# Optimization experiments

Hardware: AMD Instinct MI355X
Metric: run time of the kernel (lower is better)

Reference implementation:

```python
import jax, jax.numpy as jnp
import numpy as np

N = 100000   # nodes
E = 1600000  # directed edges
F_IN, F_HID, F_OUT = 10, 64, 4


def setup_inputs() -> dict:
    key = jax.random.key(0)
    ks = jax.random.split(key, 8)
    x = jax.random.normal(ks[0], (N, F_IN), dtype=jnp.float32)
    edge_index = jax.random.randint(ks[1], (2, E), 0, N, dtype=jnp.int64)
    W1 = jax.random.normal(ks[2], (F_IN, F_HID), dtype=jnp.float32) * (1.0 / np.sqrt(F_IN))
    b1 = jnp.zeros((F_HID,), dtype=jnp.float32)
    W2 = jax.random.normal(ks[3], (F_HID, F_HID), dtype=jnp.float32) * (1.0 / np.sqrt(F_HID))
    b2 = jnp.zeros((F_HID,), dtype=jnp.float32)
    W3 = jax.random.normal(ks[4], (F_HID, F_OUT), dtype=jnp.float32) * (1.0 / np.sqrt(F_HID))
    b3 = jnp.zeros((F_OUT,), dtype=jnp.float32)
    return {"x": x, "edge_index": edge_index, "W1": W1, "b1": b1,
            "W2": W2, "b2": b2, "W3": W3, "b3": b3}


def _gcn_layer(h_in, W, b, src, dst, dinv_sqrt):
    # GCNConv: D^{-1/2} (A + I) D^{-1/2} (h_in W) + b, with deg counted incl. self-loops
    h = h_in @ W                                   # [N, F_out]
    norm = dinv_sqrt[src] * dinv_sqrt[dst]         # [E]
    msg = h[src] * norm[:, None]                   # [E, F_out]  (dominant traffic)
    agg = jax.ops.segment_sum(msg, dst, num_segments=N)
    agg = agg + h * (dinv_sqrt * dinv_sqrt)[:, None]  # self-loop contribution
    return agg + b


def reference(x, edge_index, W1, b1, W2, b2, W3, b3):
    src, dst = edge_index[0], edge_index[1]
    # degree of target nodes including self-loop
    deg = jax.ops.segment_sum(jnp.ones((E,), x.dtype), dst, num_segments=N) + 1.0
    dinv_sqrt = jax.lax.rsqrt(deg)
    h = jax.nn.relu(_gcn_layer(x, W1, b1, src, dst, dinv_sqrt))
    # dropout is identity in eval mode (training=False)
    h = jax.nn.relu(_gcn_layer(h, W2, b2, src, dst, dinv_sqrt))
    h = _gcn_layer(h, W3, b3, src, dst, dinv_sqrt)
    return jax.nn.log_softmax(h, axis=1)
```

## Files before the change

### kernel.cpp

```cpp
#include <hip/hip_runtime.h>
#include <hip/hip_bf16.h>
#include <math.h>


#define D_MAX 48
#define BUCK_SH 7
#define NPB 128
#define NBK 782
#define P1_BLOCKS 256
#define P1_THREADS 512
#define SEG_CAP 36

typedef __hip_bfloat16 bf16;

__global__ void k_bin(const int* __restrict__ src, const int* __restrict__ dst,
                      int* __restrict__ arena, int* __restrict__ cnt2, int E) {
    __shared__ int lcnt[NBK];
    int t = threadIdx.x, blk = blockIdx.x;
    for (int i = t; i < NBK; i += P1_THREADS) lcnt[i] = 0;
    __syncthreads();
    int chunk = (E + P1_BLOCKS - 1) / P1_BLOCKS;
    int e0 = blk * chunk;
    int e1 = min(e0 + chunk, E);
    for (int e = e0 + t; e < e1; e += P1_THREADS) {
        int d = __builtin_nontemporal_load(dst + e);
        int s = __builtin_nontemporal_load(src + e);
        int b = d >> BUCK_SH;
        int rec = (d & (NPB - 1)) | (s << BUCK_SH);
        int slot = atomicAdd(&lcnt[b], 1);
        if (slot < SEG_CAP)
            arena[((size_t)b * P1_BLOCKS + blk) * SEG_CAP + slot] = rec;
    }
    __syncthreads();
    for (int b = t; b < NBK; b += P1_THREADS)
        cnt2[b * P1_BLOCKS + blk] = lcnt[b];
}

__global__ void k_ellbuild(const int* __restrict__ arena, const int* __restrict__ cnt2,
                           const float* __restrict__ x,
                           int* __restrict__ ell, int* __restrict__ cnt,
                           float* __restrict__ dinv, bf16* __restrict__ xp, int N) {
    __shared__ int cnt128[NPB];
    __shared__ int ellb[NPB * D_MAX];
    __shared__ float dloc[NPB];
    int t = threadIdx.x, b = blockIdx.x;
    if (t < NPB) cnt128[t] = 0;
    __syncthreads();
    int c = cnt2[b * P1_BLOCKS + t];
    int cc = min(c, SEG_CAP);
    const int* seg = arena + ((size_t)b * P1_BLOCKS + t) * SEG_CAP;
    for (int i = 0; i < cc; ++i) {
        int rec = seg[i];
        int r = rec & (NPB - 1);
        int s = rec >> BUCK_SH;
        int slot = atomicAdd(&cnt128[r], 1);
        if (slot < D_MAX) ellb[r * D_MAX + slot] = s;
    }
    __syncthreads();
    int nb = b << BUCK_SH;
    if (t < NPB) {
        int n = nb + t;
        if (n < N) {
            int dg = cnt128[t];
            cnt[n] = dg;
            float dv = rsqrtf((float)dg + 1.0f);
            dinv[n] = dv;
            dloc[t] = dv;
        }
    }
    __syncthreads();
    for (int i = t; i < NPB * D_MAX; i += 256) {
        int n = nb + i / D_MAX;
        if (n < N) ell[(size_t)nb * D_MAX + i] = ellb[i];
    }
    for (int i = t; i < NPB * 10; i += 256) {
        int n = nb + i / 10;
        if (n < N) xp[(size_t)nb * 10 + i] = __float2bfloat16(x[(size_t)nb * 10 + i] * dloc[i / 10]);
    }
}

__global__ void k_gather10(const int* __restrict__ ell, const int* __restrict__ cnt,
                           const bf16* __restrict__ xp, const float* __restrict__ dinv,
                           float* __restrict__ aggx, int N) {
    int tid = threadIdx.x;
    int g = tid & 15;
    int node = blockIdx.x * 16 + (tid >> 4);
    if (node >= N) return;
    int deg = cnt[node]; if (deg > D_MAX) deg = D_MAX;
    float acc = 0.0f;
    for (int c0 = 0; c0 < deg; c0 += 16) {
        int m = deg - c0; if (m > 16) m = 16;
        int sid = 0;
        if (g < m) sid = ell[(size_t)node * D_MAX + c0 + g];
        for (int i = 0; i < m; ++i) {
            int s = __shfl(sid, i, 16);
            if (g < 10) acc += __bfloat162float(xp[(size_t)s * 10 + g]);
        }
    }
    if (g < 10) {
        acc += __bfloat162float(xp[(size_t)node * 10 + g]);
        aggx[(size_t)node * 10 + g] = dinv[node] * acc;
    }
}

__global__ void k_fused1(const float* __restrict__ aggx, const float* __restrict__ W1,
                         const float* __restrict__ b1, const float* __restrict__ W2,
                         const float* __restrict__ dinv, bf16* __restrict__ t, int N) {
    __shared__ float W1s[10 * 64];
    __shared__ float h1s[64][64];
    int tid = threadIdx.x;
    int f = tid & 63, w = tid >> 6;
    float w2c[64];
#pragma unroll
    for (int k = 0; k < 64; ++k) w2c[k] = W2[k * 64 + f];
    for (int i = tid; i < 640; i += 256) W1s[i] = W1[i];
    __syncthreads();
    int nb = blockIdx.x * 64;
    float bf = b1[f];
    for (int j = 0; j < 16; ++j) {
        int ln = w * 16 + j;
        int n = nb + ln;
        float acc = bf;
        if (n < N) {
#pragma unroll
            for (int k = 0; k < 10; ++k)
                acc = fmaf(aggx[(size_t)n * 10 + k], W1s[k * 64 + f], acc);
        }
        h1s[ln][f] = fmaxf(acc, 0.0f);
    }
    __syncthreads();
    for (int j = 0; j < 16; ++j) {
        int ln = w * 16 + j;
        int n = nb + ln;
        if (n >= N) continue;
        float acc = 0.0f;
        const float4* hr = (const float4*)h1s[ln];
#pragma unroll
        for (int k4 = 0; k4 < 16; ++k4) {
            float4 h = hr[k4];
            acc = fmaf(h.x, w2c[k4 * 4 + 0], acc);
            acc = fmaf(h.y, w2c[k4 * 4 + 1], acc);
            acc = fmaf(h.z, w2c[k4 * 4 + 2], acc);
            acc = fmaf(h.w, w2c[k4 * 4 + 3], acc);
        }
        t[(size_t)n * 64 + f] = __float2bfloat16(acc * dinv[n]);
    }
}

__global__ void k_fused2(const int* __restrict__ ell, const int* __restrict__ cnt,
                         const bf16* __restrict__ t, const float* __restrict__ dinv,
                         const float* __restrict__ b2, const float* __restrict__ W3,
                         float* __restrict__ t3, int N) {
    __shared__ float W3s[256];
    int tid = threadIdx.x;
    W3s[tid] = W3[tid];
    __syncthreads();
    int f = tid & 63;
    int node = blockIdx.x * 4 + (tid >> 6);
    if (node >= N) return;
    int deg = cnt[node]; if (deg > D_MAX) deg = D_MAX;
    int sid = 0;
    if (f < deg) sid = ell[(size_t)node * D_MAX + f];
    float acc = 0.0f;
    int i = 0;
    for (; i + 4 <= deg; i += 4) {
        int s0 = __shfl(sid, i),     s1 = __shfl(sid, i + 1);
        int s2 = __shfl(sid, i + 2), s3 = __shfl(sid, i + 3);
        float v0 = __bfloat162float(t[(size_t)s0 * 64 + f]);
        float v1 = __bfloat162float(t[(size_t)s1 * 64 + f]);
        float v2 = __bfloat162float(t[(size_t)s2 * 64 + f]);
        float v3 = __bfloat162float(t[(size_t)s3 * 64 + f]);
        acc += v0 + v1;
        acc += v2 + v3;
    }
    for (; i < deg; ++i) {
        int s = __shfl(sid, i);
        acc += __bfloat162float(t[(size_t)s * 64 + f]);
    }
    float di = dinv[node];
    acc += __bfloat162float(t[(size_t)node * 64 + f]);
    float h2 = fmaxf(di * acc + b2[f], 0.0f);
    float p0 = h2 * W3s[f * 4 + 0];
    float p1 = h2 * W3s[f * 4 + 1];
    float p2 = h2 * W3s[f * 4 + 2];
    float p3 = h2 * W3s[f * 4 + 3];
#pragma unroll
    for (int off = 32; off > 0; off >>= 1) {
        p0 += __shfl_down(p0, off);
        p1 += __shfl_down(p1, off);
        p2 += __shfl_down(p2, off);
        p3 += __shfl_down(p3, off);
    }
    if (f == 0) {
        float4 r = {p0 * di, p1 * di, p2 * di, p3 * di};
        *(float4*)(t3 + (size_t)node * 4) = r;
    }
}

__global__ void k_out(const int* __restrict__ ell, const int* __restrict__ cnt,
                      const float* __restrict__ t3, const float* __restrict__ dinv,
                      const float* __restrict__ b3, float* __restrict__ out, int N) {
    int n = blockIdx.x * blockDim.x + threadIdx.x;
    if (n >= N) return;
    int deg = cnt[n]; if (deg > D_MAX) deg = D_MAX;
    float a0 = 0.f, a1 = 0.f, a2 = 0.f, a3 = 0.f;
    const int* row = ell + (size_t)n * D_MAX;
    for (int c = 0; c < deg; c += 4) {
        int4 q = *(const int4*)(row + c);
        {
            float4 v = *(const float4*)(t3 + (size_t)q.x * 4);
            a0 += v.x; a1 += v.y; a2 += v.z; a3 += v.w;
        }
        if (c + 1 < deg) {
            float4 v = *(const float4*)(t3 + (size_t)q.y * 4);
            a0 += v.x; a1 += v.y; a2 += v.z; a3 += v.w;
        }
        if (c + 2 < deg) {
            float4 v = *(const float4*)(t3 + (size_t)q.z * 4);
            a0 += v.x; a1 += v.y; a2 += v.z; a3 += v.w;
        }
        if (c + 3 < deg) {
            float4 v = *(const float4*)(t3 + (size_t)q.w * 4);
            a0 += v.x; a1 += v.y; a2 += v.z; a3 += v.w;
        }
    }
    float4 sv = *(const float4*)(t3 + (size_t)n * 4);
    a0 += sv.x; a1 += sv.y; a2 += sv.z; a3 += sv.w;
    float di = dinv[n];
    float v0 = di * a0 + b3[0];
    float v1 = di * a1 + b3[1];
    float v2 = di * a2 + b3[2];
    float v3 = di * a3 + b3[3];
    float m = fmaxf(fmaxf(v0, v1), fmaxf(v2, v3));
    float s = expf(v0 - m) + expf(v1 - m) + expf(v2 - m) + expf(v3 - m);
    float ls = m + logf(s);
    float4 r = {v0 - ls, v1 - ls, v2 - ls, v3 - ls};
    *(float4*)(out + (size_t)n * 4) = r;
}

extern "C" void kernel_launch(void* const* d_in, const int* in_sizes, int n_in,
                              void* d_out, int out_size, void* d_ws, size_t ws_size,
                              hipStream_t stream) {
    const float* x  = (const float*)d_in[0];
    const int*   ei = (const int*)d_in[1];
    const float* W1 = (const float*)d_in[2];
    const float* b1 = (const float*)d_in[3];
    const float* W2 = (const float*)d_in[4];
    const float* b2 = (const float*)d_in[5];
    const float* W3 = (const float*)d_in[6];
    const float* b3 = (const float*)d_in[7];
    float* out = (float*)d_out;

    const int E = in_sizes[1] / 2;
    const int N = in_sizes[0] / 10;
    const int* src = ei;
    const int* dst = ei + E;

    float* dinv  = (float*)d_ws;
    int*   cnt   = (int*)(dinv + N);
    int*   ell   = cnt + N;
    bf16*  xp    = (bf16*)(ell + (size_t)N * D_MAX);
    float* t3    = (float*)(xp + (size_t)N * 10 + 4);
    int*   arena = (int*)(t3 + (size_t)N * 4);
    int*   cnt2  = arena + (size_t)NBK * P1_BLOCKS * SEG_CAP;
    float* aggx  = (float*)arena;
    bf16*  tbuf  = (bf16*)(aggx + (size_t)N * 10);

    k_bin<<<P1_BLOCKS, P1_THREADS, 0, stream>>>(src, dst, arena, cnt2, E);
    k_ellbuild<<<NBK, 256, 0, stream>>>(arena, cnt2, x, ell, cnt, dinv, xp, N);

    k_gather10<<<(N + 15) / 16, 256, 0, stream>>>(ell, cnt, xp, dinv, aggx, N);
    k_fused1<<<(N + 63) / 64, 256, 0, stream>>>(aggx, W1, b1, W2, dinv, tbuf, N);
    k_fused2<<<(N + 3) / 4, 256, 0, stream>>>(ell, cnt, tbuf, dinv, b2, W3, t3, N);
    k_out<<<(N + 255) / 256, 256, 0, stream>>>(ell, cnt, t3, dinv, b3, out, N);
}
```

Before: 199.6 us.

## Fuse layer-1 gather into dense kernel, vectorize binning loads, deepen gather unroll

Merges the 10-feature neighbor gather into the layer-1/layer-2 transform kernel, so the aggregated features stay in shared memory and one launch plus the aggx round trip through global memory go away. The binning pass now reads src/dst as 4-wide vectors, and the ELL build reads segment records as int4. The layer-2 gather loop is unrolled from 4 to 8 neighbors for more memory-level parallelism. The t3 alignment padding changes, and the fused kernel may lose occupancy because the gather now runs inside a register-heavy kernel.

New measurement: 200.5 us. Within noise of the previous version (+0.4%).

```diff
diff --git a/kernel.cpp b/kernel.cpp
--- a/kernel.cpp
+++ b/kernel.cpp
@@ -12,6 +12,7 @@
 #define SEG_CAP 36
 
 typedef __hip_bfloat16 bf16;
+typedef int int4v __attribute__((ext_vector_type(4)));
 
 __global__ void k_bin(const int* __restrict__ src, const int* __restrict__ dst,
                       int* __restrict__ arena, int* __restrict__ cnt2, int E) {
@@ -19,18 +20,30 @@
     int t = threadIdx.x, blk = blockIdx.x;
     for (int i = t; i < NBK; i += P1_THREADS) lcnt[i] = 0;
     __syncthreads();
-    int chunk = (E + P1_BLOCKS - 1) / P1_BLOCKS;
-    int e0 = blk * chunk;
-    int e1 = min(e0 + chunk, E);
-    for (int e = e0 + t; e < e1; e += P1_THREADS) {
-        int d = __builtin_nontemporal_load(dst + e);
-        int s = __builtin_nontemporal_load(src + e);
-        int b = d >> BUCK_SH;
-        int rec = (d & (NPB - 1)) | (s << BUCK_SH);
-        int slot = atomicAdd(&lcnt[b], 1);
-        if (slot < SEG_CAP)
-            arena[((size_t)b * P1_BLOCKS + blk) * SEG_CAP + slot] = rec;
-    }
+#define BIN_ONE(d_, s_) {                                                   \
+        int b_ = (d_) >> BUCK_SH;                                           \
+        int rec_ = ((d_) & (NPB - 1)) | ((s_) << BUCK_SH);                  \
+        int slot_ = atomicAdd(&lcnt[b_], 1);                                \
+        if (slot_ < SEG_CAP)                                                \
+            arena[((size_t)b_ * P1_BLOCKS + blk) * SEG_CAP + slot_] = rec_; \
+    }
+    int E4 = E >> 2;
+    int chunk4 = (E4 + P1_BLOCKS - 1) / P1_BLOCKS;
+    int q0 = blk * chunk4;
+    int q1 = min(q0 + chunk4, E4);
+    for (int q = q0 + t; q < q1; q += P1_THREADS) {
+        int4v d4 = __builtin_nontemporal_load((const int4v*)dst + q);
+        int4v s4 = __builtin_nontemporal_load((const int4v*)src + q);
+        BIN_ONE(d4.x, s4.x);
+        BIN_ONE(d4.y, s4.y);
+        BIN_ONE(d4.z, s4.z);
+        BIN_ONE(d4.w, s4.w);
+    }
+    if (blk == 0 && t < (E & 3)) {
+        int e = (E & ~3) + t;
+        BIN_ONE(dst[e], src[e]);
+    }
+#undef BIN_ONE
     __syncthreads();
     for (int b = t; b < NBK; b += P1_THREADS)
         cnt2[b * P1_BLOCKS + blk] = lcnt[b];
@@ -48,14 +61,22 @@
     __syncthreads();
     int c = cnt2[b * P1_BLOCKS + t];
     int cc = min(c, SEG_CAP);
-    const int* seg = arena + ((size_t)b * P1_BLOCKS + t) * SEG_CAP;
-    for (int i = 0; i < cc; ++i) {
-        int rec = seg[i];
-        int r = rec & (NPB - 1);
-        int s = rec >> BUCK_SH;
-        int slot = atomicAdd(&cnt128[r], 1);
-        if (slot < D_MAX) ellb[r * D_MAX + slot] = s;
-    }
+#define INS_ONE(rec_) {                                                     \
+        int r_ = (rec_) & (NPB - 1);                                        \
+        int s_ = (rec_) >> BUCK_SH;                                         \
+        int slot_ = atomicAdd(&cnt128[r_], 1);                              \
+        if (slot_ < D_MAX) ellb[r_ * D_MAX + slot_] = s_;                   \
+    }
+    const int4v* segv = (const int4v*)(arena + ((size_t)b * P1_BLOCKS + t) * SEG_CAP);
+    for (int i4 = 0; i4 * 4 < cc; ++i4) {
+        int4v r4 = segv[i4];
+        int lim = cc - i4 * 4;
+        INS_ONE(r4.x);
+        if (lim > 1) INS_ONE(r4.y);
+        if (lim > 2) INS_ONE(r4.z);
+        if (lim > 3) INS_ONE(r4.w);
+    }
+#undef INS_ONE
     __syncthreads();
     int nb = b << BUCK_SH;
     if (t < NPB) {
@@ -79,34 +100,12 @@
     }
 }
 
-__global__ void k_gather10(const int* __restrict__ ell, const int* __restrict__ cnt,
-                           const bf16* __restrict__ xp, const float* __restrict__ dinv,
-                           float* __restrict__ aggx, int N) {
-    int tid = threadIdx.x;
-    int g = tid & 15;
-    int node = blockIdx.x * 16 + (tid >> 4);
-    if (node >= N) return;
-    int deg = cnt[node]; if (deg > D_MAX) deg = D_MAX;
-    float acc = 0.0f;
-    for (int c0 = 0; c0 < deg; c0 += 16) {
-        int m = deg - c0; if (m > 16) m = 16;
-        int sid = 0;
-        if (g < m) sid = ell[(size_t)node * D_MAX + c0 + g];
-        for (int i = 0; i < m; ++i) {
-            int s = __shfl(sid, i, 16);
-            if (g < 10) acc += __bfloat162float(xp[(size_t)s * 10 + g]);
-        }
-    }
-    if (g < 10) {
-        acc += __bfloat162float(xp[(size_t)node * 10 + g]);
-        aggx[(size_t)node * 10 + g] = dinv[node] * acc;
-    }
-}
-
-__global__ void k_fused1(const float* __restrict__ aggx, const float* __restrict__ W1,
-                         const float* __restrict__ b1, const float* __restrict__ W2,
-                         const float* __restrict__ dinv, bf16* __restrict__ t, int N) {
+__global__ void k_fused1(const int* __restrict__ ell, const int* __restrict__ cnt,
+                         const bf16* __restrict__ xp, const float* __restrict__ dinv,
+                         const float* __restrict__ W1, const float* __restrict__ b1,
+                         const float* __restrict__ W2, bf16* __restrict__ t, int N) {
     __shared__ float W1s[10 * 64];
+    __shared__ float aggxs[64][10];
     __shared__ float h1s[64][64];
     int tid = threadIdx.x;
     int f = tid & 63, w = tid >> 6;
@@ -114,18 +113,37 @@
 #pragma unroll
     for (int k = 0; k < 64; ++k) w2c[k] = W2[k * 64 + f];
     for (int i = tid; i < 640; i += 256) W1s[i] = W1[i];
-    __syncthreads();
     int nb = blockIdx.x * 64;
+    int g = tid & 15;
+    for (int pass = 0; pass < 4; ++pass) {
+        int ln = pass * 16 + (tid >> 4);
+        int node = nb + ln;
+        if (node < N) {
+            int deg = cnt[node]; if (deg > D_MAX) deg = D_MAX;
+            float acc = 0.0f;
+            for (int c0 = 0; c0 < deg; c0 += 16) {
+                int m = deg - c0; if (m > 16) m = 16;
+                int sid = 0;
+                if (g < m) sid = ell[(size_t)node * D_MAX + c0 + g];
+                for (int i = 0; i < m; ++i) {
+                    int s = __shfl(sid, i, 16);
+                    if (g < 10) acc += __bfloat162float(xp[(size_t)s * 10 + g]);
+                }
+            }
+            if (g < 10) {
+                acc += __bfloat162float(xp[(size_t)node * 10 + g]);
+                aggxs[ln][g] = dinv[node] * acc;
+            }
+        }
+    }
+    __syncthreads();
     float bf = b1[f];
     for (int j = 0; j < 16; ++j) {
         int ln = w * 16 + j;
-        int n = nb + ln;
         float acc = bf;
-        if (n < N) {
-#pragma unroll
-            for (int k = 0; k < 10; ++k)
-                acc = fmaf(aggx[(size_t)n * 10 + k], W1s[k * 64 + f], acc);
-        }
+#pragma unroll
+        for (int k = 0; k < 10; ++k)
+            acc = fmaf(aggxs[ln][k], W1s[k * 64 + f], acc);
         h1s[ln][f] = fmaxf(acc, 0.0f);
     }
     __syncthreads();
@@ -163,15 +181,20 @@
     if (f < deg) sid = ell[(size_t)node * D_MAX + f];
     float acc = 0.0f;
     int i = 0;
-    for (; i + 4 <= deg; i += 4) {
+    for (; i + 8 <= deg; i += 8) {
         int s0 = __shfl(sid, i),     s1 = __shfl(sid, i + 1);
         int s2 = __shfl(sid, i + 2), s3 = __shfl(sid, i + 3);
+        int s4 = __shfl(sid, i + 4), s5 = __shfl(sid, i + 5);
+        int s6 = __shfl(sid, i + 6), s7 = __shfl(sid, i + 7);
         float v0 = __bfloat162float(t[(size_t)s0 * 64 + f]);
         float v1 = __bfloat162float(t[(size_t)s1 * 64 + f]);
         float v2 = __bfloat162float(t[(size_t)s2 * 64 + f]);
         float v3 = __bfloat162float(t[(size_t)s3 * 64 + f]);
-        acc += v0 + v1;
-        acc += v2 + v3;
+        float v4 = __bfloat162float(t[(size_t)s4 * 64 + f]);
+        float v5 = __bfloat162float(t[(size_t)s5 * 64 + f]);
+        float v6 = __bfloat162float(t[(size_t)s6 * 64 + f]);
+        float v7 = __bfloat162float(t[(size_t)s7 * 64 + f]);
+        acc += ((v0 + v1) + (v2 + v3)) + ((v4 + v5) + (v6 + v7));
     }
     for (; i < deg; ++i) {
         int s = __shfl(sid, i);
@@ -260,17 +283,15 @@
     int*   cnt   = (int*)(dinv + N);
     int*   ell   = cnt + N;
     bf16*  xp    = (bf16*)(ell + (size_t)N * D_MAX);
-    float* t3    = (float*)(xp + (size_t)N * 10 + 4);
+    float* t3    = (float*)(xp + (size_t)N * 10 + 8);
     int*   arena = (int*)(t3 + (size_t)N * 4);
     int*   cnt2  = arena + (size_t)NBK * P1_BLOCKS * SEG_CAP;
-    float* aggx  = (float*)arena;
-    bf16*  tbuf  = (bf16*)(aggx + (size_t)N * 10);
+    bf16*  tbuf  = (bf16*)arena;
 
     k_bin<<<P1_BLOCKS, P1_THREADS, 0, stream>>>(src, dst, arena, cnt2, E);
     k_ellbuild<<<NBK, 256, 0, stream>>>(arena, cnt2, x, ell, cnt, dinv, xp, N);
 
-    k_gather10<<<(N + 15) / 16, 256, 0, stream>>>(ell, cnt, xp, dinv, aggx, N);
-    k_fused1<<<(N + 63) / 64, 256, 0, stream>>>(aggx, W1, b1, W2, dinv, tbuf, N);
+    k_fused1<<<(N + 63) / 64, 256, 0, stream>>>(ell, cnt, xp, dinv, W1, b1, W2, tbuf, N);
     k_fused2<<<(N + 3) / 4, 256, 0, stream>>>(ell, cnt, tbuf, dinv, b2, W3, t3, N);
     k_out<<<(N + 255) / 256, 256, 0, stream>>>(ell, cnt, t3, dinv, b3, out, N);
 }
```
